# Kernel tuning notes

Hardware: AMD Instinct MI355X
Metric: run time of the kernel (lower is better)

The kernel has to match this reference:

```python
import jax, jax.numpy as jnp
import numpy as np

L, B, S, D, H, V = 6, 4, 1024, 1024, 16, 32000
HD = D // H          # head_size = 64
F = 4 * D            # ffn hidden
EPS = 1e-5           # nn.LayerNorm default


def setup_inputs() -> dict:
    key = jax.random.key(0)
    ks = jax.random.split(key, 12)
    s = 0.02
    p = {
        "tokens": jax.random.randint(ks[0], (B, S), 0, V, dtype=jnp.int32),
        "tok_emb": s * jax.random.normal(ks[1], (V, D), jnp.float32),
        "pos_emb": s * jax.random.normal(ks[2], (S, D), jnp.float32),
        # stacked per-layer params (leading dim L)
        "Wq": s * jax.random.normal(ks[3], (L, D, D), jnp.float32),
        "Wk": s * jax.random.normal(ks[4], (L, D, D), jnp.float32),
        "Wv": s * jax.random.normal(ks[5], (L, D, D), jnp.float32),
        "Wp": s * jax.random.normal(ks[6], (L, D, D), jnp.float32),
        "ln1_s": jnp.ones((L, D), jnp.float32),
        "ln1_b": jnp.zeros((L, D), jnp.float32),
        "W1": s * jax.random.normal(ks[7], (L, D, F), jnp.float32),
        "b1": jnp.zeros((L, F), jnp.float32),
        "W2": s * jax.random.normal(ks[8], (L, F, D), jnp.float32),
        "b2": jnp.zeros((L, D), jnp.float32),
        "ln2_s": jnp.ones((L, D), jnp.float32),
        "ln2_b": jnp.zeros((L, D), jnp.float32),
        "lnf_s": jnp.ones((D,), jnp.float32),
        "lnf_b": jnp.zeros((D,), jnp.float32),
        "Wh": s * jax.random.normal(ks[9], (D, V), jnp.float32),
        "bh": jnp.zeros((V,), jnp.float32),
    }
    return p


def _ln(x, scale, bias):
    m = x.mean(-1, keepdims=True)
    v = ((x - m) ** 2).mean(-1, keepdims=True)
    return (x - m) * jax.lax.rsqrt(v + EPS) * scale + bias


def reference(tokens, tok_emb, pos_emb, Wq, Wk, Wv, Wp, ln1_s, ln1_b,
              W1, b1, W2, b2, ln2_s, ln2_b, lnf_s, lnf_b, Wh, bh):
    x = tok_emb[tokens] + pos_emb[None, :, :]            # [B,S,D]
    mask = jnp.tril(jnp.ones((S, S), dtype=bool))
    inv_sqrt_hd = HD ** -0.5

    def layer(x, p):
        wq, wk, wv, wp, l1s, l1b, w1, b1_, w2, b2_, l2s, l2b = p
        q = jnp.einsum('bsd,dhk->bhsk', x, wq.reshape(D, H, HD))
        k = jnp.einsum('bsd,dhk->bhsk', x, wk.reshape(D, H, HD))
        v = jnp.einsum('bsd,dhk->bhsk', x, wv.reshape(D, H, HD))
        scores = jnp.einsum('bhsk,bhtk->bhst', q, k)     # [B,H,S,S]
        # original: masked_fill(-inf) THEN * head_size**-0.5 (same math: -inf stays -inf)
        scores = jnp.where(mask, scores * inv_sqrt_hd, -jnp.inf)
        attn = jax.nn.softmax(scores, axis=-1)
        o = jnp.einsum('bhst,bhtk->bhsk', attn, v)
        o = o.transpose(0, 2, 1, 3).reshape(B, S, D) @ wp
        a = x + _ln(o, l1s, l1b)                          # residual + ln1 (as in source)
        f = jax.nn.relu(a @ w1 + b1_) @ w2 + b2_
        return x + _ln(f, l2s, l2b), None                 # residual from block INPUT (as in source)

    x, _ = jax.lax.scan(layer, x,
                        (Wq, Wk, Wv, Wp, ln1_s, ln1_b, W1, b1, W2, b2, ln2_s, ln2_b))
    return _ln(x, lnf_s, lnf_b) @ Wh + bh                 # [B,S,V]
```

## Files before the change

kernel.cpp:

```cpp
#include <hip/hip_runtime.h>

#define DEV __device__ __forceinline__

typedef __attribute__((ext_vector_type(4))) float f32x4;
typedef __attribute__((ext_vector_type(8))) short short8_t;

constexpr int LNUM = 6;
constexpr int BB = 4;
constexpr int SS = 1024;
constexpr int DD = 1024;
constexpr int HH = 16;
constexpr int HDD = 64;
constexpr int FF = 4096;
constexpr int VV = 32000;
constexpr int MROWS = BB * SS;

DEV short f2bf(float f) {
  union { float f; unsigned u; } x; x.f = f;
  unsigned r = x.u + 0x7fffu + ((x.u >> 16) & 1u);
  return (short)(r >> 16);
}

#define BAR() do { __builtin_amdgcn_sched_barrier(0); \
  __builtin_amdgcn_s_barrier(); \
  __builtin_amdgcn_sched_barrier(0); } while (0)

__global__ __launch_bounds__(256) void k_embed(
    const int* __restrict__ tok, const float* __restrict__ te,
    const float* __restrict__ pe, float* __restrict__ xf,
    short* __restrict__ xb) {
  int i = blockIdx.x * 256 + threadIdx.x;
  int bs = i >> 8, d4 = i & 255;
  int t = tok[bs];
  float4 a = ((const float4*)(te + (size_t)t * DD))[d4];
  float4 b = ((const float4*)(pe + (size_t)(bs & (SS - 1)) * DD))[d4];
  float4 r; r.x = a.x + b.x; r.y = a.y + b.y; r.z = a.z + b.z; r.w = a.w + b.w;
  ((float4*)xf)[i] = r;
  short4 o; o.x = f2bf(r.x); o.y = f2bf(r.y); o.z = f2bf(r.z); o.w = f2bf(r.w);
  ((short4*)xb)[i] = o;
}

__global__ __launch_bounds__(256) void k_tcvt(
    const float* __restrict__ in, short* __restrict__ out, int K, int N,
    long long ostride) {
  __shared__ float tile[32][33];
  const float* ip = in + (size_t)blockIdx.z * K * N;
  short* op = out + (size_t)blockIdx.z * ostride;
  int bn = blockIdx.x * 32, bk = blockIdx.y * 32;
  int tx = threadIdx.x, ty = threadIdx.y;
  #pragma unroll
  for (int r = 0; r < 32; r += 8)
    tile[ty + r][tx] = ip[(size_t)(bk + ty + r) * N + bn + tx];
  __syncthreads();
  #pragma unroll
  for (int r = 0; r < 32; r += 8)
    op[(size_t)(bn + ty + r) * K + bk + tx] = f2bf(tile[tx][ty + r]);
}

DEV void gload16(const short* g, short* l) {
  __builtin_amdgcn_global_load_lds(
      (const __attribute__((address_space(1))) void*)g,
      (__attribute__((address_space(3))) void*)l, 16, 0, 0);
}

template<int MODE>
__global__ __launch_bounds__(512, 2) void k_gemm256(
    const short* __restrict__ A, const short* __restrict__ Bt,
    const float* __restrict__ bias, void* __restrict__ Cp,
    int M, int N, int K, int lda, int ldb) {
  extern __shared__ short lds[];
  const int tid = threadIdx.x;
  const int nbx = gridDim.x;
  const int nwg = nbx << 4;
  const int hid = blockIdx.y * nbx + blockIdx.x;
  const int cpx = nwg >> 3;
  const int lid = (hid & 7) * cpx + (hid >> 3);
  const int bx = lid >> 4, by = lid & 15;
  const int n0 = bx * 256, m0 = by * 256;

  const int lane = tid & 63;
  const int wid = tid >> 6;
  const int wm = wid >> 2, wn = wid & 3;
  const int l16 = lane & 15, kg = lane >> 4;
  const int xorv = (l16 & 7) << 4;
  const int cs[2] = { ((kg << 4) ^ xorv) >> 1,
                      ((64 | (kg << 4)) ^ xorv) >> 1 };
  const int rr = tid >> 3;
  const int sce = ((((tid & 7) << 4) ^ ((rr & 7) << 4)) >> 1);
  const int ldst = (tid & ~63) * 8;

  const int NT = K >> 6;

  auto stageA = [&](int t2, int c2) {
    const int k0 = t2 << 6;
    const int base = c2 * 32768;
    #pragma unroll
    for (int h = 0; h < 2; h++)
      #pragma unroll
      for (int li = 0; li < 2; li++)
        gload16(A + (size_t)(m0 + h * 128 + li * 64 + rr) * lda + k0 + sce,
                &lds[base + h * 8192 + li * 4096 + ldst]);
  };
  auto stageB = [&](int t2, int c2) {
    const int k0 = t2 << 6;
    const int base = c2 * 32768 + 16384;
    #pragma unroll
    for (int h = 0; h < 2; h++)
      #pragma unroll
      for (int li = 0; li < 2; li++)
        gload16(Bt + (size_t)(n0 + h * 128 + li * 64 + rr) * ldb + k0 + sce,
                &lds[base + h * 8192 + li * 4096 + ldst]);
  };

  f32x4 acc[8][4];
  #pragma unroll
  for (int mi = 0; mi < 8; mi++)
    #pragma unroll
    for (int ni = 0; ni < 4; ni++)
      #pragma unroll
      for (int j = 0; j < 4; j++) acc[mi][ni][j] = 0.f;

  auto storeQ = [&](int mlo, int nlo) {
    #pragma unroll
    for (int mi = 0; mi < 4; mi++)
      #pragma unroll
      for (int ni = 0; ni < 2; ni++)
        #pragma unroll
        for (int j = 0; j < 4; j++) {
          const int r = m0 + wm * 128 + (mlo + mi) * 16 + kg * 4 + j;
          const int c = n0 + wn * 64 + (nlo + ni) * 16 + l16;
          ((float*)Cp)[(size_t)r * N + c] = acc[mlo + mi][nlo + ni][j] + bias[c];
        }
  };

  stageA(0, 0); stageB(0, 0);
  stageA(1, 1); stageB(1, 1);
  asm volatile("s_waitcnt vmcnt(8)" ::: "memory");
  BAR();

  for (int t = 0; t < NT; t++) {
    const int c = t & 1;
    const int ao = c * 32768 + wm * 8192;
    const int bo = c * 32768 + 16384 + (wn >> 1) * 8192 + (wn & 1) * 4096;
    short8_t a[4][2], b0[2][2], b1[2][2];

    #pragma unroll
    for (int mi = 0; mi < 4; mi++)
      #pragma unroll
      for (int kk = 0; kk < 2; kk++)
        a[mi][kk] = *(const short8_t*)&lds[ao + (mi * 16 + l16) * 64 + cs[kk]];
    #pragma unroll
    for (int ni = 0; ni < 2; ni++)
      #pragma unroll
      for (int kk = 0; kk < 2; kk++)
        b0[ni][kk] = *(const short8_t*)&lds[bo + (ni * 16 + l16) * 64 + cs[kk]];
    BAR();
    __builtin_amdgcn_s_setprio(1);
    #pragma unroll
    for (int mi = 0; mi < 4; mi++)
      #pragma unroll
      for (int ni = 0; ni < 2; ni++)
        #pragma unroll
        for (int kk = 0; kk < 2; kk++)
          acc[mi][ni] = __builtin_amdgcn_mfma_f32_16x16x32_bf16(
              a[mi][kk], b0[ni][kk], acc[mi][ni], 0, 0, 0);
    __builtin_amdgcn_s_setprio(0);
    if (MODE == 9 && t == NT - 1) storeQ(0, 0);
    BAR();

    #pragma unroll
    for (int ni = 0; ni < 2; ni++)
      #pragma unroll
      for (int kk = 0; kk < 2; kk++)
        b1[ni][kk] = *(const short8_t*)&lds[bo + ((ni + 2) * 16 + l16) * 64 + cs[kk]];
    BAR();
    __builtin_amdgcn_s_setprio(1);
    #pragma unroll
    for (int mi = 0; mi < 4; mi++)
      #pragma unroll
      for (int ni = 0; ni < 2; ni++)
        #pragma unroll
        for (int kk = 0; kk < 2; kk++)
          acc[mi][ni + 2] = __builtin_amdgcn_mfma_f32_16x16x32_bf16(
              a[mi][kk], b1[ni][kk], acc[mi][ni + 2], 0, 0, 0);
    __builtin_amdgcn_s_setprio(0);
    if (MODE == 9 && t == NT - 1) storeQ(0, 2);
    BAR();

    #pragma unroll
    for (int mi = 0; mi < 4; mi++)
      #pragma unroll
      for (int kk = 0; kk < 2; kk++)
        a[mi][kk] = *(const short8_t*)&lds[ao + ((mi + 4) * 16 + l16) * 64 + cs[kk]];
    if (t + 2 < NT) stageB(t + 2, c);
    BAR();
    __builtin_amdgcn_s_setprio(1);
    #pragma unroll
    for (int mi = 0; mi < 4; mi++)
      #pragma unroll
      for (int ni = 0; ni < 2; ni++)
        #pragma unroll
        for (int kk = 0; kk < 2; kk++)
          acc[mi + 4][ni + 2] = __builtin_amdgcn_mfma_f32_16x16x32_bf16(
              a[mi][kk], b1[ni][kk], acc[mi + 4][ni + 2], 0, 0, 0);
    __builtin_amdgcn_s_setprio(0);
    if (MODE == 9 && t == NT - 1) storeQ(4, 2);
    BAR();

    if (t + 2 < NT) stageA(t + 2, c);
    BAR();
    __builtin_amdgcn_s_setprio(1);
    #pragma unroll
    for (int mi = 0; mi < 4; mi++)
      #pragma unroll
      for (int ni = 0; ni < 2; ni++)
        #pragma unroll
        for (int kk = 0; kk < 2; kk++)
          acc[mi + 4][ni] = __builtin_amdgcn_mfma_f32_16x16x32_bf16(
              a[mi][kk], b0[ni][kk], acc[mi + 4][ni], 0, 0, 0);
    __builtin_amdgcn_s_setprio(0);
    if (t + 2 < NT) asm volatile("s_waitcnt vmcnt(8)" ::: "memory");
    else            asm volatile("s_waitcnt vmcnt(0)" ::: "memory");
    BAR();
  }

  if (MODE == 9) {
    storeQ(4, 0);
    return;
  }
  #pragma unroll
  for (int mi = 0; mi < 8; mi++) {
    #pragma unroll
    for (int ni = 0; ni < 4; ni++) {
      #pragma unroll
      for (int j = 0; j < 4; j++) {
        const int r = m0 + wm * 128 + mi * 16 + kg * 4 + j;
        const int c = n0 + wn * 64 + ni * 16 + l16;
        const float v = acc[mi][ni][j];
        if (MODE == 6) {
          ((short*)Cp)[(size_t)r * N + c] = f2bf(fmaxf(v + bias[c], 0.f));
        } else if (MODE == 8) {
          int kind = c >> 10, cc = c & 1023;
          int b = r >> 10, s = r & 1023, h = cc >> 6, hd = cc & 63;
          size_t off;
          if (kind < 2)
            off = (size_t)kind * MROWS * DD +
                  (((size_t)(b * HH + h) << 10) + s) * HDD + hd;
          else
            off = (size_t)2 * MROWS * DD +
                  (((size_t)(b * HH + h) * HDD + hd) << 10) + s;
          ((short*)Cp)[off] = f2bf(v);
        }
      }
    }
  }
}

template<int MODE>
__global__ __launch_bounds__(256) void k_gemm(
    const short* __restrict__ A, const short* __restrict__ Bt,
    const float* __restrict__ bias, void* __restrict__ Cp,
    int M, int N, int K, int lda, int ldb) {
  __shared__ short lA[4096];
  __shared__ short lB[4096];
  const int tid = threadIdx.x;
  const int n0 = blockIdx.x * 128, m0 = blockIdx.y * 128;

  const int lane = tid & 63;
  const int wm = (tid >> 6) >> 1, wn = (tid >> 6) & 1;
  const int l16 = lane & 15, kg = lane >> 4;
  const int srow = tid >> 2, scol = (tid & 3) * 8;
  const int lbase = (tid & ~63) * 8;

  f32x4 acc[4][4];
  #pragma unroll
  for (int a = 0; a < 4; a++)
    #pragma unroll
    for (int b = 0; b < 4; b++)
      #pragma unroll
      for (int j = 0; j < 4; j++) acc[a][b][j] = 0.f;

  for (int k0 = 0; k0 < K; k0 += 32) {
    #pragma unroll
    for (int i = 0; i < 2; i++)
      gload16(A + (size_t)(m0 + i * 64 + srow) * lda + (k0 + scol),
              &lA[i * 2048 + lbase]);
    #pragma unroll
    for (int i = 0; i < 2; i++)
      gload16(Bt + (size_t)(n0 + i * 64 + srow) * ldb + (k0 + scol),
              &lB[i * 2048 + lbase]);
    __syncthreads();
    short8_t af[4], bf[4];
    #pragma unroll
    for (int mi = 0; mi < 4; mi++)
      af[mi] = *(const short8_t*)&lA[(wm * 64 + mi * 16 + l16) * 32 + kg * 8];
    #pragma unroll
    for (int ni = 0; ni < 4; ni++)
      bf[ni] = *(const short8_t*)&lB[(wn * 64 + ni * 16 + l16) * 32 + kg * 8];
    #pragma unroll
    for (int mi = 0; mi < 4; mi++)
      #pragma unroll
      for (int ni = 0; ni < 4; ni++)
        acc[mi][ni] = __builtin_amdgcn_mfma_f32_16x16x32_bf16(
            af[mi], bf[ni], acc[mi][ni], 0, 0, 0);
    __syncthreads();
  }

  #pragma unroll
  for (int mi = 0; mi < 4; mi++) {
    #pragma unroll
    for (int ni = 0; ni < 4; ni++) {
      #pragma unroll
      for (int j = 0; j < 4; j++) {
        const int r = m0 + wm * 64 + mi * 16 + kg * 4 + j;
        const int c = n0 + wn * 64 + ni * 16 + l16;
        const float v = acc[mi][ni][j];
        if (MODE == 5) {
          ((float*)Cp)[(size_t)r * N + c] = v;
        } else if (MODE == 7) {
          ((float*)Cp)[(size_t)r * N + c] = v + bias[c];
        }
      }
    }
  }
}

#define RDSWZ(arr, r, cb) \
  (*(const short8_t*)&arr[((r) << 6) + ((((cb) ^ (((r) & 7) << 4))) >> 1)])
#define RDSWZ7(arr, r, cb) \
  (*(const short8_t*)&arr[((r) << 7) + ((((cb) ^ (((r) & 7) << 4))) >> 1)])

__global__ __launch_bounds__(256, 2) void k_attn(
    const short* __restrict__ Qg, const short* __restrict__ Kgl,
    const short* __restrict__ Vt, short* __restrict__ Og) {
  extern __shared__ short sm[];
  short* lQ = sm;
  short* lK = sm + 8192;
  short* lV = sm + 16384;
  short* lP = sm + 24576;
  const int tid = threadIdx.x;
  const int z = blockIdx.y;
  const int qb = (z < 32) ? blockIdx.x : 7 - blockIdx.x;
  const int q0 = qb << 7;
  const short* Qp = Qg + ((size_t)z << 16);
  const short* Kp = Kgl + ((size_t)z << 16);
  const short* Vp = Vt + ((size_t)z << 16);
  const int bidx = z >> 4, h = z & 15;
  const int lane = tid & 63, w = tid >> 6;
  const int l16 = lane & 15, kg = lane >> 4;
  const int sr = tid >> 3;
  const int scb = ((((tid & 7) << 4) ^ ((sr & 7) << 4)) >> 1);
  const int vr = tid >> 4;
  const int vcb = ((((tid & 15) << 4) ^ ((vr & 7) << 4)) >> 1);
  const int ldst = (tid & ~63) << 3;

  #pragma unroll
  for (int i = 0; i < 4; i++)
    gload16(Qp + ((size_t)(q0 + i * 32 + sr) << 6) + scb, &lQ[i * 2048 + ldst]);

  f32x4 acc_o[2][4];
  float m_r[2][4], l_r[2][4];
  #pragma unroll
  for (int mi = 0; mi < 2; mi++)
    #pragma unroll
    for (int j = 0; j < 4; j++) {
      m_r[mi][j] = -3e38f; l_r[mi][j] = 0.f;
      #pragma unroll
      for (int n2 = 0; n2 < 4; n2++) acc_o[mi][n2][j] = 0.f;
    }

  const int nkt = qb + 1;
  for (int kt = 0; kt < nkt; kt++) {
    const int k0 = kt << 7;
    #pragma unroll
    for (int i = 0; i < 4; i++)
      gload16(Kp + ((size_t)(k0 + i * 32 + sr) << 6) + scb, &lK[i * 2048 + ldst]);
    #pragma unroll
    for (int i = 0; i < 4; i++)
      gload16(Vp + ((size_t)(i * 16 + vr) << 10) + k0 + vcb, &lV[i * 2048 + ldst]);
    __syncthreads();

    f32x4 s[2][8];
    #pragma unroll
    for (int mi = 0; mi < 2; mi++)
      #pragma unroll
      for (int nf = 0; nf < 8; nf++)
        #pragma unroll
        for (int j = 0; j < 4; j++) s[mi][nf][j] = 0.f;
    #pragma unroll
    for (int kk = 0; kk < 2; kk++) {
      short8_t aq[2];
      #pragma unroll
      for (int mi = 0; mi < 2; mi++)
        aq[mi] = RDSWZ(lQ, w * 32 + mi * 16 + l16, kk * 64 + kg * 16);
      #pragma unroll
      for (int nf = 0; nf < 8; nf++) {
        short8_t bk = RDSWZ(lK, nf * 16 + l16, kk * 64 + kg * 16);
        #pragma unroll
        for (int mi = 0; mi < 2; mi++)
          s[mi][nf] = __builtin_amdgcn_mfma_f32_16x16x32_bf16(
              aq[mi], bk, s[mi][nf], 0, 0, 0);
      }
    }

    const bool diag = (kt == qb);
    #pragma unroll
    for (int mi = 0; mi < 2; mi++) {
      #pragma unroll
      for (int j = 0; j < 4; j++) {
        const int ql = w * 32 + mi * 16 + kg * 4 + j;
        const int q = q0 + ql;
        float sv[8]; float tm = -3e38f;
        #pragma unroll
        for (int nf = 0; nf < 8; nf++) {
          int kv = k0 + nf * 16 + l16;
          sv[nf] = (!diag || kv <= q) ? s[mi][nf][j] * 0.125f : -3e38f;
          tm = fmaxf(tm, sv[nf]);
        }
        #pragma unroll
        for (int o = 1; o < 16; o <<= 1) tm = fmaxf(tm, __shfl_xor(tm, o));
        const float mn = fmaxf(m_r[mi][j], tm);
        const float scale = __expf(m_r[mi][j] - mn);
        float e[8]; float ts = 0.f;
        #pragma unroll
        for (int nf = 0; nf < 8; nf++) { e[nf] = __expf(sv[nf] - mn); ts += e[nf]; }
        #pragma unroll
        for (int o = 1; o < 16; o <<= 1) ts += __shfl_xor(ts, o);
        l_r[mi][j] = l_r[mi][j] * scale + ts;
        m_r[mi][j] = mn;
        #pragma unroll
        for (int n2 = 0; n2 < 4; n2++) acc_o[mi][n2][j] *= scale;
        #pragma unroll
        for (int nf = 0; nf < 8; nf++)
          lP[(ql << 7) + ((nf * 16 + l16) ^ ((ql & 7) << 3))] = f2bf(e[nf]);
      }
    }

    #pragma unroll
    for (int kc = 0; kc < 4; kc++) {
      short8_t pa[2];
      #pragma unroll
      for (int mi = 0; mi < 2; mi++) {
        const int pr = w * 32 + mi * 16 + l16;
        pa[mi] = *(const short8_t*)
            &lP[(pr << 7) + ((kc * 32 + kg * 8) ^ ((pr & 7) << 3))];
      }
      #pragma unroll
      for (int n2 = 0; n2 < 4; n2++) {
        short8_t vb = RDSWZ7(lV, n2 * 16 + l16, kc * 64 + kg * 16);
        #pragma unroll
        for (int mi = 0; mi < 2; mi++)
          acc_o[mi][n2] = __builtin_amdgcn_mfma_f32_16x16x32_bf16(
              pa[mi], vb, acc_o[mi][n2], 0, 0, 0);
      }
    }
    __syncthreads();
  }

  #pragma unroll
  for (int mi = 0; mi < 2; mi++) {
    #pragma unroll
    for (int j = 0; j < 4; j++) {
      const int q = q0 + w * 32 + mi * 16 + kg * 4 + j;
      const float inv = 1.f / l_r[mi][j];
      #pragma unroll
      for (int n2 = 0; n2 < 4; n2++) {
        const int col = h * HDD + n2 * 16 + l16;
        Og[(((size_t)bidx << 10) + q) * DD + col] = f2bf(acc_o[mi][n2][j] * inv);
      }
    }
  }
}

template<int ADD_RES, int WRITE_F32>
__global__ __launch_bounds__(256) void k_ln(
    const float* __restrict__ src, const float* __restrict__ res,
    const float* __restrict__ g, const float* __restrict__ b,
    float* __restrict__ of, short* __restrict__ ob) {
  const int row = blockIdx.x;
  const int tid = threadIdx.x;
  float4 v = ((const float4*)(src + ((size_t)row << 10)))[tid];
  float s1 = v.x + v.y + v.z + v.w;
  float s2 = v.x * v.x + v.y * v.y + v.z * v.z + v.w * v.w;
  #pragma unroll
  for (int o = 32; o; o >>= 1) { s1 += __shfl_xor(s1, o); s2 += __shfl_xor(s2, o); }
  __shared__ float sh1[4], sh2[4];
  if ((tid & 63) == 0) { sh1[tid >> 6] = s1; sh2[tid >> 6] = s2; }
  __syncthreads();
  s1 = sh1[0] + sh1[1] + sh1[2] + sh1[3];
  s2 = sh2[0] + sh2[1] + sh2[2] + sh2[3];
  const float mean = s1 * (1.f / 1024.f);
  const float var  = s2 * (1.f / 1024.f) - mean * mean;
  const float rs = rsqrtf(var + 1e-5f);
  float4 gg = ((const float4*)g)[tid];
  float4 bb = ((const float4*)b)[tid];
  float4 o4;
  o4.x = (v.x - mean) * rs * gg.x + bb.x;
  o4.y = (v.y - mean) * rs * gg.y + bb.y;
  o4.z = (v.z - mean) * rs * gg.z + bb.z;
  o4.w = (v.w - mean) * rs * gg.w + bb.w;
  if (ADD_RES) {
    float4 rr = ((const float4*)(res + ((size_t)row << 10)))[tid];
    o4.x += rr.x; o4.y += rr.y; o4.z += rr.z; o4.w += rr.w;
  }
  if (WRITE_F32) ((float4*)(of + ((size_t)row << 10)))[tid] = o4;
  short4 s4; s4.x = f2bf(o4.x); s4.y = f2bf(o4.y);
  s4.z = f2bf(o4.z); s4.w = f2bf(o4.w);
  ((short4*)ob)[((size_t)row << 8) + tid] = s4;
}

extern "C" void kernel_launch(void* const* d_in, const int* in_sizes, int n_in,
                              void* d_out, int out_size, void* d_ws, size_t ws_size,
                              hipStream_t stream) {
  (void)in_sizes; (void)n_in; (void)out_size; (void)ws_size;
  const int*   tokens  = (const int*)d_in[0];
  const float* tok_emb = (const float*)d_in[1];
  const float* pos_emb = (const float*)d_in[2];
  const float* Wq = (const float*)d_in[3];
  const float* Wk = (const float*)d_in[4];
  const float* Wv = (const float*)d_in[5];
  const float* Wp = (const float*)d_in[6];
  const float* ln1s = (const float*)d_in[7];
  const float* ln1b = (const float*)d_in[8];
  const float* W1 = (const float*)d_in[9];
  const float* b1 = (const float*)d_in[10];
  const float* W2 = (const float*)d_in[11];
  const float* b2 = (const float*)d_in[12];
  const float* ln2s = (const float*)d_in[13];
  const float* ln2b = (const float*)d_in[14];
  const float* lnfs = (const float*)d_in[15];
  const float* lnfb = (const float*)d_in[16];
  const float* Wh = (const float*)d_in[17];
  const float* bh = (const float*)d_in[18];
  float* out = (float*)d_out;

  hipFuncSetAttribute((const void*)k_gemm256<6>,
      hipFuncAttributeMaxDynamicSharedMemorySize, 131072);
  hipFuncSetAttribute((const void*)k_gemm256<8>,
      hipFuncAttributeMaxDynamicSharedMemorySize, 131072);
  hipFuncSetAttribute((const void*)k_gemm256<9>,
      hipFuncAttributeMaxDynamicSharedMemorySize, 131072);
  hipFuncSetAttribute((const void*)k_attn,
      hipFuncAttributeMaxDynamicSharedMemorySize, 81920);

  char* p = (char*)d_ws;
  auto alloc = [&](size_t elems, size_t esz) -> char* {
    char* r = p; p += (elems * esz + 255) & ~(size_t)255; return r;
  };
  short* WqkvT = (short*)alloc((size_t)LNUM * 3 * DD * DD, 2);
  short* WpT = (short*)alloc((size_t)LNUM * DD * DD, 2);
  short* W1T = (short*)alloc((size_t)LNUM * DD * FF, 2);
  short* W2T = (short*)alloc((size_t)LNUM * DD * FF, 2);
  short* WhT = (short*)alloc((size_t)DD * VV, 2);
  float* xf   = (float*)alloc((size_t)MROWS * DD, 4);
  float* ff   = (float*)alloc((size_t)MROWS * DD, 4);
  short* xb   = (short*)alloc((size_t)MROWS * DD, 2);
  short* ab   = (short*)alloc((size_t)MROWS * DD, 2);
  short* qkvb = (short*)alloc((size_t)3 * MROWS * DD, 2);
  short* obuf = (short*)alloc((size_t)MROWS * DD, 2);
  short* hb   = (short*)alloc((size_t)MROWS * FF, 2);
  short* xfb  = (short*)alloc((size_t)MROWS * DD, 2);
  short* qb   = qkvb;
  short* kb   = qkvb + (size_t)MROWS * DD;
  short* vtb  = qkvb + (size_t)2 * MROWS * DD;

  dim3 blk(256);
  dim3 t8(32, 8);
  const long long DD2 = (long long)DD * DD;
  k_tcvt<<<dim3(DD / 32, DD / 32, LNUM), t8, 0, stream>>>(Wq, WqkvT,          DD, DD, 3 * DD2);
  k_tcvt<<<dim3(DD / 32, DD / 32, LNUM), t8, 0, stream>>>(Wk, WqkvT + DD2,    DD, DD, 3 * DD2);
  k_tcvt<<<dim3(DD / 32, DD / 32, LNUM), t8, 0, stream>>>(Wv, WqkvT + 2*DD2,  DD, DD, 3 * DD2);
  k_tcvt<<<dim3(DD / 32, DD / 32, LNUM), t8, 0, stream>>>(Wp, WpT, DD, DD, DD2);
  k_tcvt<<<dim3(FF / 32, DD / 32, LNUM), t8, 0, stream>>>(W1, W1T, DD, FF, (long long)DD * FF);
  k_tcvt<<<dim3(DD / 32, FF / 32, LNUM), t8, 0, stream>>>(W2, W2T, FF, DD, (long long)DD * FF);
  k_tcvt<<<dim3(VV / 32, DD / 32, 1),   t8, 0, stream>>>(Wh, WhT, DD, VV, 0);

  k_embed<<<(MROWS * DD / 4) / 256, blk, 0, stream>>>(tokens, tok_emb, pos_emb, xf, xb);

  for (int l = 0; l < LNUM; l++) {
    const short* wqkv = WqkvT + (size_t)l * 3 * DD * DD;
    const short* wp = WpT + (size_t)l * DD * DD;
    const short* w1 = W1T + (size_t)l * DD * FF;
    const short* w2 = W2T + (size_t)l * DD * FF;

    k_gemm256<8><<<dim3(12, 16), 512, 131072, stream>>>(xb, wqkv, nullptr, qkvb,
        MROWS, 3 * DD, DD, DD, DD);
    k_attn<<<dim3(8, BB * HH), blk, 81920, stream>>>(qb, kb, vtb, obuf);
    k_gemm<5><<<dim3(8, 32), blk, 0, stream>>>(obuf, wp, nullptr, ff,
        MROWS, DD, DD, DD, DD);
    k_ln<1, 0><<<MROWS, blk, 0, stream>>>(ff, xf, ln1s + (size_t)l * DD,
        ln1b + (size_t)l * DD, nullptr, ab);
    k_gemm256<6><<<dim3(16, 16), 512, 131072, stream>>>(ab, w1, b1 + (size_t)l * FF, hb,
        MROWS, FF, DD, DD, DD);
    k_gemm<7><<<dim3(8, 32), blk, 0, stream>>>(hb, w2, b2 + (size_t)l * DD, ff,
        MROWS, DD, FF, FF, FF);
    k_ln<1, 1><<<MROWS, blk, 0, stream>>>(ff, xf, ln2s + (size_t)l * DD,
        ln2b + (size_t)l * DD, xf, xb);
  }

  k_ln<0, 0><<<MROWS, blk, 0, stream>>>(xf, nullptr, lnfs, lnfb, nullptr, xfb);
  k_gemm256<9><<<dim3(VV / 256, 16), 512, 131072, stream>>>(xfb, WhT, bh, out,
      MROWS, VV, DD, DD, DD);
}
```

Before: 2.418 ms.

## Double-buffer K/V tiles in attention and use 8 waves of 16 query rows

The attention kernel now runs 512 threads per block, each wave owning 16 query rows instead of 32. K and V tiles are double-buffered in shared memory so the next tile's global loads are issued while the current tile is computed, with explicit vmcnt waits. Q fragments are held in registers for the whole loop. Softmax uses exp2 with the log2e factor folded into the scale. This needs more shared memory per block (96KB) and reuses the Q staging area as the second buffer, which may limit how many blocks fit on a CU.

```diff
diff --git a/kernel.cpp b/kernel.cpp
--- a/kernel.cpp
+++ b/kernel.cpp
@@ -330,14 +330,11 @@
 #define RDSWZ7(arr, r, cb) \
   (*(const short8_t*)&arr[((r) << 7) + ((((cb) ^ (((r) & 7) << 4))) >> 1)])
 
-__global__ __launch_bounds__(256, 2) void k_attn(
+__global__ __launch_bounds__(512, 2) void k_attn(
     const short* __restrict__ Qg, const short* __restrict__ Kgl,
     const short* __restrict__ Vt, short* __restrict__ Og) {
   extern __shared__ short sm[];
-  short* lQ = sm;
-  short* lK = sm + 8192;
-  short* lV = sm + 16384;
-  short* lP = sm + 24576;
+  short* lP = sm + 32768;
   const int tid = threadIdx.x;
   const int z = blockIdx.y;
   const int qb = (z < 32) ? blockIdx.x : 7 - blockIdx.x;
@@ -354,120 +351,128 @@
   const int vcb = ((((tid & 15) << 4) ^ ((vr & 7) << 4)) >> 1);
   const int ldst = (tid & ~63) << 3;
 
-  #pragma unroll
-  for (int i = 0; i < 4; i++)
-    gload16(Qp + ((size_t)(q0 + i * 32 + sr) << 6) + scb, &lQ[i * 2048 + ldst]);
-
-  f32x4 acc_o[2][4];
-  float m_r[2][4], l_r[2][4];
-  #pragma unroll
-  for (int mi = 0; mi < 2; mi++)
-    #pragma unroll
-    for (int j = 0; j < 4; j++) {
-      m_r[mi][j] = -3e38f; l_r[mi][j] = 0.f;
-      #pragma unroll
-      for (int n2 = 0; n2 < 4; n2++) acc_o[mi][n2][j] = 0.f;
+  auto stageK = [&](int kt, int c) {
+    const int k0 = kt << 7;
+    short* dst = sm + c * 16384;
+    #pragma unroll
+    for (int i = 0; i < 2; i++)
+      gload16(Kp + ((size_t)(k0 + i * 64 + sr) << 6) + scb,
+              dst + i * 4096 + ldst);
+  };
+  auto stageV = [&](int kt, int c) {
+    const int k0 = kt << 7;
+    short* dst = sm + c * 16384 + 8192;
+    #pragma unroll
+    for (int i = 0; i < 2; i++)
+      gload16(Vp + ((size_t)(i * 32 + vr) << 10) + k0 + vcb,
+              dst + i * 4096 + ldst);
+  };
+
+  #pragma unroll
+  for (int i = 0; i < 2; i++)
+    gload16(Qp + ((size_t)(q0 + i * 64 + sr) << 6) + scb,
+            sm + 16384 + i * 4096 + ldst);
+  __syncthreads();
+  short8_t aq[2];
+  #pragma unroll
+  for (int kk = 0; kk < 2; kk++)
+    aq[kk] = RDSWZ((sm + 16384), w * 16 + l16, kk * 64 + kg * 16);
+  __syncthreads();
+
+  f32x4 acc_o[4];
+  float m_r[4], l_r[4];
+  #pragma unroll
+  for (int j = 0; j < 4; j++) {
+    m_r[j] = -3e38f; l_r[j] = 0.f;
+    #pragma unroll
+    for (int n2 = 0; n2 < 4; n2++) acc_o[n2][j] = 0.f;
+  }
+
+  const float C = 0.125f * 1.44269504f;
+  const int nkt = qb + 1;
+  stageK(0, 0); stageV(0, 0);
+
+  for (int kt = 0; kt < nkt; kt++) {
+    const int cur = kt & 1;
+    if (kt + 1 < nkt) {
+      stageK(kt + 1, cur ^ 1); stageV(kt + 1, cur ^ 1);
+      asm volatile("s_waitcnt vmcnt(4)" ::: "memory");
+    } else {
+      asm volatile("s_waitcnt vmcnt(0)" ::: "memory");
     }
-
-  const int nkt = qb + 1;
-  for (int kt = 0; kt < nkt; kt++) {
+    BAR();
+
+    const short* lK = sm + cur * 16384;
+    const short* lV = sm + cur * 16384 + 8192;
     const int k0 = kt << 7;
-    #pragma unroll
-    for (int i = 0; i < 4; i++)
-      gload16(Kp + ((size_t)(k0 + i * 32 + sr) << 6) + scb, &lK[i * 2048 + ldst]);
-    #pragma unroll
-    for (int i = 0; i < 4; i++)
-      gload16(Vp + ((size_t)(i * 16 + vr) << 10) + k0 + vcb, &lV[i * 2048 + ldst]);
-    __syncthreads();
-
-    f32x4 s[2][8];
-    #pragma unroll
-    for (int mi = 0; mi < 2; mi++)
-      #pragma unroll
-      for (int nf = 0; nf < 8; nf++)
-        #pragma unroll
-        for (int j = 0; j < 4; j++) s[mi][nf][j] = 0.f;
-    #pragma unroll
-    for (int kk = 0; kk < 2; kk++) {
-      short8_t aq[2];
-      #pragma unroll
-      for (int mi = 0; mi < 2; mi++)
-        aq[mi] = RDSWZ(lQ, w * 32 + mi * 16 + l16, kk * 64 + kg * 16);
+
+    f32x4 s[8];
+    #pragma unroll
+    for (int nf = 0; nf < 8; nf++)
+      #pragma unroll
+      for (int j = 0; j < 4; j++) s[nf][j] = 0.f;
+    #pragma unroll
+    for (int kk = 0; kk < 2; kk++)
       #pragma unroll
       for (int nf = 0; nf < 8; nf++) {
         short8_t bk = RDSWZ(lK, nf * 16 + l16, kk * 64 + kg * 16);
-        #pragma unroll
-        for (int mi = 0; mi < 2; mi++)
-          s[mi][nf] = __builtin_amdgcn_mfma_f32_16x16x32_bf16(
-              aq[mi], bk, s[mi][nf], 0, 0, 0);
+        s[nf] = __builtin_amdgcn_mfma_f32_16x16x32_bf16(aq[kk], bk, s[nf], 0, 0, 0);
+      }
+
+    const bool diag = (kt == qb);
+    #pragma unroll
+    for (int j = 0; j < 4; j++) {
+      const int ql = w * 16 + kg * 4 + j;
+      const int q = q0 + ql;
+      float sv[8]; float tm = -3e38f;
+      #pragma unroll
+      for (int nf = 0; nf < 8; nf++) {
+        const int kv = k0 + nf * 16 + l16;
+        const float x = s[nf][j] * C;
+        sv[nf] = (!diag || kv <= q) ? x : -3e38f;
+        tm = fmaxf(tm, sv[nf]);
+      }
+      #pragma unroll
+      for (int o = 1; o < 16; o <<= 1) tm = fmaxf(tm, __shfl_xor(tm, o));
+      const float mn = fmaxf(m_r[j], tm);
+      const float scale = exp2f(m_r[j] - mn);
+      float ts = 0.f;
+      #pragma unroll
+      for (int nf = 0; nf < 8; nf++) {
+        const float e = exp2f(sv[nf] - mn);
+        ts += e;
+        lP[(ql << 7) + ((nf * 16 + l16) ^ ((ql & 7) << 3))] = f2bf(e);
+      }
+      #pragma unroll
+      for (int o = 1; o < 16; o <<= 1) ts += __shfl_xor(ts, o);
+      l_r[j] = l_r[j] * scale + ts;
+      m_r[j] = mn;
+      #pragma unroll
+      for (int n2 = 0; n2 < 4; n2++) acc_o[n2][j] *= scale;
+    }
+
+    #pragma unroll
+    for (int kc = 0; kc < 4; kc++) {
+      const int pr = w * 16 + l16;
+      short8_t pa = *(const short8_t*)
+          &lP[(pr << 7) + ((kc * 32 + kg * 8) ^ ((pr & 7) << 3))];
+      #pragma unroll
+      for (int n2 = 0; n2 < 4; n2++) {
+        short8_t vb = RDSWZ7(lV, n2 * 16 + l16, kc * 64 + kg * 16);
+        acc_o[n2] = __builtin_amdgcn_mfma_f32_16x16x32_bf16(pa, vb, acc_o[n2], 0, 0, 0);
       }
     }
-
-    const bool diag = (kt == qb);
-    #pragma unroll
-    for (int mi = 0; mi < 2; mi++) {
-      #pragma unroll
-      for (int j = 0; j < 4; j++) {
-        const int ql = w * 32 + mi * 16 + kg * 4 + j;
-        const int q = q0 + ql;
-        float sv[8]; float tm = -3e38f;
-        #pragma unroll
-        for (int nf = 0; nf < 8; nf++) {
-          int kv = k0 + nf * 16 + l16;
-          sv[nf] = (!diag || kv <= q) ? s[mi][nf][j] * 0.125f : -3e38f;
-          tm = fmaxf(tm, sv[nf]);
-        }
-        #pragma unroll
-        for (int o = 1; o < 16; o <<= 1) tm = fmaxf(tm, __shfl_xor(tm, o));
-        const float mn = fmaxf(m_r[mi][j], tm);
-        const float scale = __expf(m_r[mi][j] - mn);
-        float e[8]; float ts = 0.f;
-        #pragma unroll
-        for (int nf = 0; nf < 8; nf++) { e[nf] = __expf(sv[nf] - mn); ts += e[nf]; }
-        #pragma unroll
-        for (int o = 1; o < 16; o <<= 1) ts += __shfl_xor(ts, o);
-        l_r[mi][j] = l_r[mi][j] * scale + ts;
-        m_r[mi][j] = mn;
-        #pragma unroll
-        for (int n2 = 0; n2 < 4; n2++) acc_o[mi][n2][j] *= scale;
-        #pragma unroll
-        for (int nf = 0; nf < 8; nf++)
-          lP[(ql << 7) + ((nf * 16 + l16) ^ ((ql & 7) << 3))] = f2bf(e[nf]);
-      }
-    }
-
-    #pragma unroll
-    for (int kc = 0; kc < 4; kc++) {
-      short8_t pa[2];
-      #pragma unroll
-      for (int mi = 0; mi < 2; mi++) {
-        const int pr = w * 32 + mi * 16 + l16;
-        pa[mi] = *(const short8_t*)
-            &lP[(pr << 7) + ((kc * 32 + kg * 8) ^ ((pr & 7) << 3))];
-      }
-      #pragma unroll
-      for (int n2 = 0; n2 < 4; n2++) {
-        short8_t vb = RDSWZ7(lV, n2 * 16 + l16, kc * 64 + kg * 16);
-        #pragma unroll
-        for (int mi = 0; mi < 2; mi++)
-          acc_o[mi][n2] = __builtin_amdgcn_mfma_f32_16x16x32_bf16(
-              pa[mi], vb, acc_o[mi][n2], 0, 0, 0);
-      }
-    }
-    __syncthreads();
-  }
-
-  #pragma unroll
-  for (int mi = 0; mi < 2; mi++) {
-    #pragma unroll
-    for (int j = 0; j < 4; j++) {
-      const int q = q0 + w * 32 + mi * 16 + kg * 4 + j;
-      const float inv = 1.f / l_r[mi][j];
-      #pragma unroll
-      for (int n2 = 0; n2 < 4; n2++) {
-        const int col = h * HDD + n2 * 16 + l16;
-        Og[(((size_t)bidx << 10) + q) * DD + col] = f2bf(acc_o[mi][n2][j] * inv);
-      }
+    BAR();
+  }
+
+  #pragma unroll
+  for (int j = 0; j < 4; j++) {
+    const int q = q0 + w * 16 + kg * 4 + j;
+    const float inv = 1.f / l_r[j];
+    #pragma unroll
+    for (int n2 = 0; n2 < 4; n2++) {
+      const int col = h * HDD + n2 * 16 + l16;
+      Og[(((size_t)bidx << 10) + q) * DD + col] = f2bf(acc_o[n2][j] * inv);
     }
   }
 }
@@ -541,7 +546,7 @@
   hipFuncSetAttribute((const void*)k_gemm256<9>,
       hipFuncAttributeMaxDynamicSharedMemorySize, 131072);
   hipFuncSetAttribute((const void*)k_attn,
-      hipFuncAttributeMaxDynamicSharedMemorySize, 81920);
+      hipFuncAttributeMaxDynamicSharedMemorySize, 98304);
 
   char* p = (char*)d_ws;
   auto alloc = [&](size_t elems, size_t esz) -> char* {
@@ -585,7 +590,7 @@
 
     k_gemm256<8><<<dim3(12, 16), 512, 131072, stream>>>(xb, wqkv, nullptr, qkvb,
         MROWS, 3 * DD, DD, DD, DD);
-    k_attn<<<dim3(8, BB * HH), blk, 81920, stream>>>(qb, kb, vtb, obuf);
+    k_attn<<<dim3(8, BB * HH), 512, 98304, stream>>>(qb, kb, vtb, obuf);
     k_gemm<5><<<dim3(8, 32), blk, 0, stream>>>(obuf, wp, nullptr, ff,
         MROWS, DD, DD, DD, DD);
     k_ln<1, 0><<<MROWS, blk, 0, stream>>>(ff, xf, ln1s + (size_t)l * DD,
```

New measurement: 2.398 ms. About the same (-0.8%).
